# Performance work log

Measured on AMD Instinct MI355X. Metric: run time of the kernel, lower is better.

## Reference

```python
import jax, jax.numpy as jnp
import numpy as np

B, NG, H, G, T0, T1 = 4096, 3000, 6, 30, 500, 50  # batch, genes, hidden, genes/term, leaf terms, mid terms
EPS = 1e-5  # BatchNorm1d default eps


def _bn(x, gamma, beta):
    # training-mode BatchNorm1d: biased batch stats over the batch axis
    m = x.mean(axis=0)
    v = ((x - m) ** 2).mean(axis=0)
    return gamma * (x - m) / jnp.sqrt(v + EPS) + beta


def setup_inputs() -> dict:
    key = jax.random.key(0)
    ks = iter(jax.random.split(key, 32))
    rn = lambda shape, s=0.05: jax.random.normal(next(ks), shape, dtype=jnp.float32) * s
    return dict(
        cell_features=jax.random.normal(next(ks), (B, NG), dtype=jnp.float32),
        Wdg=rn((T0 + T1 + 1, G, NG)), bdg=rn((T0 + T1 + 1, G)),
        W0=rn((T0, H, G)), b0=rn((T0, H)), gam0=jnp.ones((T0, H), jnp.float32), bet0=jnp.zeros((T0, H), jnp.float32),
        aw0=rn((T0, H)), ab0=rn((T0,)), av0=rn((T0,)), ac0=rn((T0,)),
        W1=rn((T1, H, 10 * H + G)), b1=rn((T1, H)), gam1=jnp.ones((T1, H), jnp.float32), bet1=jnp.zeros((T1, H), jnp.float32),
        aw1=rn((T1, H)), ab1=rn((T1,)), av1=rn((T1,)), ac1=rn((T1,)),
        W2=rn((H, T1 * H + G)), b2=rn((H,)), gam2=jnp.ones((H,), jnp.float32), bet2=jnp.zeros((H,), jnp.float32),
        aw2=rn((H,)), ab2=rn(()), av2=rn(()), ac2=rn(()),
    )


def reference(cell_features, Wdg, bdg,
              W0, b0, gam0, bet0, aw0, ab0, av0, ac0,
              W1, b1, gam1, bet1, aw1, ab1, av1, ac1,
              W2, b2, gam2, bet2, aw2, ab2, av2, ac2):
    # direct_gene_layer for every term: Linear(ngene -> genes_per_term), no activation
    dg = jnp.einsum('bn,tgn->btg', cell_features, Wdg) + bdg  # [B, 551, G]
    # ---- layer 0 (leaves): input = direct gene output only ----
    z0 = jnp.tanh(jnp.einsum('btg,thg->bth', dg[:, :T0], W0) + b0)
    n0 = _bn(z0, gam0, bet0)                                   # [B, T0, H]
    aux0 = jnp.tanh(jnp.einsum('bth,th->bt', n0, aw0) + ab0) * av0 + ac0
    # ---- layer 1: term t's children are leaves [10t, 10t+10); concat children + direct genes ----
    in1 = jnp.concatenate([n0.reshape(B, T1, 10 * H), dg[:, T0:T0 + T1]], axis=-1)  # [B, T1, 90]
    z1 = jnp.tanh(jnp.einsum('bti,thi->bth', in1, W1) + b1)
    n1 = _bn(z1, gam1, bet1)                                   # [B, T1, H]
    aux1 = jnp.tanh(jnp.einsum('bth,th->bt', n1, aw1) + ab1) * av1 + ac1
    # ---- root: children = all mid terms + direct genes ----
    in2 = jnp.concatenate([n1.reshape(B, T1 * H), dg[:, -1]], axis=-1)  # [B, 330]
    z2 = jnp.tanh(in2 @ W2.T + b2)
    n2 = _bn(z2, gam2, bet2)                                   # [B, H]
    aux2 = jnp.tanh(n2 @ aw2 + ab2) * av2 + ac2                # [B]
    # flatten (aux_out_map, term_NN_out_map) into one array for a single comparable output
    aux_all = jnp.concatenate([aux0, aux1, aux2[:, None]], axis=1)              # [B, 551]
    nn_all = jnp.concatenate([n0.reshape(B, -1), n1.reshape(B, -1), n2], axis=1)  # [B, 551*H]
    return jnp.concatenate([aux_all, nn_all], axis=1)          # [B, 3857]
```

## Files before the change

kernel.cpp:

```cpp
#include <hip/hip_runtime.h>
#include <hip/hip_bf16.h>

#define BATCH 4096
#define NGENE 3000
#define HID   6
#define GPT   30
#define T0N   500
#define T1N   50
#define KP    3008
#define MROWS 4608
#define OUTW  3857
#define BNEPS 1e-5f

typedef __attribute__((ext_vector_type(8))) __bf16 bf16x8;
typedef __attribute__((ext_vector_type(4))) float f32x4;
typedef __attribute__((ext_vector_type(8))) unsigned short ushort8;

__device__ __forceinline__ unsigned short f2bf(float f) {
  unsigned int u = __builtin_bit_cast(unsigned int, f);
  u = (u + 0x7fffu + ((u >> 16) & 1u)) >> 16;
  return (unsigned short)u;
}

__device__ __forceinline__ void gload_lds16(const void* g, void* l) {
  __builtin_amdgcn_global_load_lds(
      (const __attribute__((address_space(1))) unsigned int*)g,
      (__attribute__((address_space(3))) unsigned int*)l, 16, 0, 0);
}

__device__ __forceinline__ void bn_ss(const float* __restrict__ st,
                                      const float* __restrict__ gam,
                                      const float* __restrict__ bet,
                                      int c, float& sc, float& sh) {
  float m = st[2 * c] * (1.f / BATCH);
  float v = st[2 * c + 1] * (1.f / BATCH) - m * m;
  sc = gam[c] * rsqrtf(v + BNEPS);
  sh = bet[c] - m * sc;
}

__global__ __launch_bounds__(256) void prep(
    const float* __restrict__ cell, const float* __restrict__ Wdg,
    const float* __restrict__ W0, const float* __restrict__ b0,
    const float* __restrict__ bdg,
    ushort8* __restrict__ cellb, unsigned short* __restrict__ abuf,
    float* __restrict__ bias, float* __restrict__ st) {
  int blk = blockIdx.x, tid = threadIdx.x;
  if (blk < 6016) {
    int idx = blk * 256 + tid;
    int r = idx / 376, c8 = idx - r * 376;
    int c = c8 * 8;
    ushort8 o = (ushort8)0;
    if (c < NGENE) {
      const float4* p = (const float4*)(cell + (size_t)r * NGENE + c);
      float4 a = p[0], b = p[1];
      o[0] = f2bf(a.x); o[1] = f2bf(a.y); o[2] = f2bf(a.z); o[3] = f2bf(a.w);
      o[4] = f2bf(b.x); o[5] = f2bf(b.y); o[6] = f2bf(b.z); o[7] = f2bf(b.w);
    }
    cellb[idx] = o;
  } else if (blk < 12016) {
    int bx = blk - 6016;
    int xb = bx % 12, t = bx / 12;
    int n = xb * 256 + tid;
    if (n >= KP) return;
    bool valid = n < NGENE;
    float x[GPT];
#pragma unroll
    for (int g = 0; g < GPT; ++g)
      x[g] = valid ? Wdg[((size_t)(t * GPT + g)) * NGENE + n] : 0.f;
#pragma unroll
    for (int h = 0; h < HID; ++h) {
      const float* w = W0 + (t * HID + h) * GPT;
      float s = 0.f;
#pragma unroll
      for (int g = 0; g < GPT; ++g) s += x[g] * w[g];
      abuf[((size_t)(t * HID + h)) * KP + n] = valid ? f2bf(s) : (unsigned short)0;
    }
  } else if (blk < 14264) {
    int idx = (blk - 12016) * 256 + tid;
    if (idx >= 1530 * 376) return;
    int r = idx / 376, c8 = idx - r * 376;
    int c = c8 * 8;
    ushort8 o = (ushort8)0;
    if (c < NGENE) {
      const float4* p = (const float4*)(Wdg + (size_t)(15000 + r) * NGENE + c);
      float4 a = p[0], b = p[1];
      o[0] = f2bf(a.x); o[1] = f2bf(a.y); o[2] = f2bf(a.z); o[3] = f2bf(a.w);
      o[4] = f2bf(b.x); o[5] = f2bf(b.y); o[6] = f2bf(b.z); o[7] = f2bf(b.w);
    }
    ((ushort8*)abuf)[(size_t)(3000 + r) * 376 + c8] = o;
  } else if (blk < 14379) {
    int idx = (blk - 14264) * 256 + tid;
    if (idx < 78 * 376) ((ushort8*)abuf)[(size_t)4530 * 376 + idx] = (ushort8)0;
  } else if (blk < 14397) {
    int idx = (blk - 14379) * 256 + tid;
    if (idx >= MROWS) return;
    float v = 0.f;
    if (idx < 3000) {
      int t = idx / HID;
      float s = b0[idx];
#pragma unroll
      for (int g = 0; g < GPT; ++g) s += W0[idx * GPT + g] * bdg[t * GPT + g];
      v = s;
    } else if (idx < 4530) {
      v = bdg[15000 + idx - 3000];
    }
    bias[idx] = v;
  } else {
    int idx = (blk - 14397) * 256 + tid;
    if (idx < 6612) st[idx] = 0.f;
  }
}

__global__ __launch_bounds__(256) void gemm_fused(
    const unsigned short* __restrict__ A,
    const unsigned short* __restrict__ Bt,
    const float* __restrict__ bias,
    float* __restrict__ C,
    float* __restrict__ st0) {
  __shared__ unsigned short smem[8192];
  const int tid  = threadIdx.x;
  const int wave = tid >> 6, lane = tid & 63;
  const int wm = wave >> 1, wn = wave & 1;
  const int quad = lane >> 4, fr = lane & 15;
  const int m0 = blockIdx.y * 128, n0 = blockIdx.x * 128;
  const int lrow = lane >> 2;
  const int lcol = (lane & 3) * 8;

  f32x4 acc[16] = {};

  for (int kt = 0; kt < KP / 32; ++kt) {
    const int k0 = kt * 32;
#pragma unroll
    for (int q = 0; q < 4; ++q) {
      int chunk = q * 4 + wave;
      const unsigned short* gsrc;
      if (chunk < 8) {
        int row = m0 + chunk * 16 + lrow;
        gsrc = A + (size_t)row * KP + k0 + lcol;
      } else {
        int row = n0 + (chunk - 8) * 16 + lrow;
        gsrc = Bt + (size_t)row * KP + k0 + lcol;
      }
      gload_lds16(gsrc, &smem[chunk * 512]);
    }
    asm volatile("s_waitcnt vmcnt(0)" ::: "memory");
    __syncthreads();

    bf16x8 af[4], bfr[4];
#pragma unroll
    for (int tm = 0; tm < 4; ++tm)
      af[tm] = ((const bf16x8*)smem)[((wm * 64 + tm * 16 + fr) * 32 + quad * 8) >> 3];
#pragma unroll
    for (int tn = 0; tn < 4; ++tn)
      bfr[tn] = ((const bf16x8*)smem)[(4096 + (wn * 64 + tn * 16 + fr) * 32 + quad * 8) >> 3];
#pragma unroll
    for (int tm = 0; tm < 4; ++tm)
#pragma unroll
      for (int tn = 0; tn < 4; ++tn)
        acc[tm * 4 + tn] = __builtin_amdgcn_mfma_f32_16x16x32_bf16(
            af[tm], bfr[tn], acc[tm * 4 + tn], 0, 0, 0);
    __syncthreads();
  }

#pragma unroll
  for (int tm = 0; tm < 4; ++tm) {
    const int mbase = m0 + wm * 64 + tm * 16 + quad * 4;
    float s1[4] = {0.f, 0.f, 0.f, 0.f}, s2[4] = {0.f, 0.f, 0.f, 0.f};
#pragma unroll
    for (int tn = 0; tn < 4; ++tn) {
      int n = n0 + wn * 64 + tn * 16 + fr;
#pragma unroll
      for (int r = 0; r < 4; ++r) {
        int m = mbase + r;
        float v = acc[tm * 4 + tn][r] + bias[m];
        if (m < 3000) {
          v = tanhf(v);
          s1[r] += v; s2[r] += v * v;
        }
        C[(size_t)m * BATCH + n] = v;
      }
    }
#pragma unroll
    for (int r = 0; r < 4; ++r) {
      int m = mbase + r;
      if (m < 3000) {
        float a = s1[r], q = s2[r];
        a += __shfl_xor(a, 1);  q += __shfl_xor(q, 1);
        a += __shfl_xor(a, 2);  q += __shfl_xor(q, 2);
        a += __shfl_xor(a, 4);  q += __shfl_xor(q, 4);
        a += __shfl_xor(a, 8);  q += __shfl_xor(q, 8);
        if (fr == 0) {
          atomicAdd(&st0[2 * m], a);
          atomicAdd(&st0[2 * m + 1], q);
        }
      }
    }
  }
}

__device__ void norm_emit_body(const float* __restrict__ zT, const float* __restrict__ st,
                               const float* __restrict__ gam, const float* __restrict__ bet,
                               float* __restrict__ out, int ncols, int outoff,
                               int xb, int yb) {
  __shared__ float tile[64][65];
  int lane = threadIdx.x & 63, w = threadIdx.x >> 6;
  int c0 = xb * 64, b0 = yb * 64;
#pragma unroll
  for (int i = 0; i < 16; ++i) {
    int cc = w * 16 + i, c = c0 + cc;
    float n = 0.f;
    if (c < ncols) {
      float sc, sh; bn_ss(st, gam, bet, c, sc, sh);
      n = zT[(size_t)c * BATCH + b0 + lane] * sc + sh;
    }
    tile[cc][lane] = n;
  }
  __syncthreads();
  int c = c0 + lane;
  if (c < ncols) {
#pragma unroll
    for (int i = 0; i < 16; ++i) {
      int rr = w * 16 + i;
      out[(size_t)(b0 + rr) * OUTW + outoff + c] = tile[lane][rr];
    }
  }
}

__global__ __launch_bounds__(256) void fused_l1(
    const float* __restrict__ C, const float* __restrict__ st0,
    const float* __restrict__ gam0, const float* __restrict__ bet0,
    const float* __restrict__ aw0, const float* __restrict__ ab0,
    const float* __restrict__ av0, const float* __restrict__ ac0,
    const float* __restrict__ W1, const float* __restrict__ b1,
    float* __restrict__ out, float* __restrict__ auxT,
    float* __restrict__ z1T, float* __restrict__ st1) {
  int blk = blockIdx.x;
  if (blk < 3008) {
    norm_emit_body(C, st0, gam0, bet0, out, 3000, 551, blk % 47, blk / 47);
  } else if (blk < 11008) {
    int b2 = blk - 3008;
    int lane = threadIdx.x & 63, tg = threadIdx.x >> 6;
    int t = (b2 % 125) * 4 + tg;
    int b = (b2 / 125) * 64 + lane;
    float s = ab0[t];
#pragma unroll
    for (int h = 0; h < HID; ++h) {
      int c = t * HID + h;
      float sc, sh; bn_ss(st0, gam0, bet0, c, sc, sh);
      s += (C[(size_t)c * BATCH + b] * sc + sh) * aw0[c];
    }
    auxT[(size_t)t * BATCH + b] = tanhf(s) * av0[t] + ac0[t];
  } else {
    int b3 = blk - 11008;
    int lane = threadIdx.x & 63, tg = threadIdx.x >> 6;
    int t = (b3 % 13) * 4 + tg;
    if (t >= T1N) return;
    int b = (b3 / 13) * 64 + lane;
    const float* dgm = C + (size_t)3000 * BATCH;
    float x[90];
#pragma unroll
    for (int j = 0; j < 60; ++j) {
      int c = t * 60 + j;
      float sc, sh; bn_ss(st0, gam0, bet0, c, sc, sh);
      x[j] = C[(size_t)c * BATCH + b] * sc + sh;
    }
#pragma unroll
    for (int g = 0; g < GPT; ++g)
      x[60 + g] = dgm[(size_t)(t * GPT + g) * BATCH + b];
#pragma unroll
    for (int h = 0; h < HID; ++h) {
      int c = t * HID + h;
      const float* w = W1 + c * 90;
      float s = b1[c];
#pragma unroll
      for (int i = 0; i < 90; ++i) s += x[i] * w[i];
      float z = tanhf(s);
      z1T[(size_t)c * BATCH + b] = z;
      float s1 = z, s2 = z * z;
#pragma unroll
      for (int off = 32; off > 0; off >>= 1) {
        s1 += __shfl_down(s1, off);
        s2 += __shfl_down(s2, off);
      }
      if (lane == 0) {
        atomicAdd(&st1[2 * c], s1);
        atomicAdd(&st1[2 * c + 1], s2);
      }
    }
  }
}

__global__ __launch_bounds__(256) void fused_l2(
    const float* __restrict__ C, const float* __restrict__ z1T,
    const float* __restrict__ st1,
    const float* __restrict__ gam1, const float* __restrict__ bet1,
    const float* __restrict__ aw1, const float* __restrict__ ab1,
    const float* __restrict__ av1, const float* __restrict__ ac1,
    const float* __restrict__ W2, const float* __restrict__ b2,
    float* __restrict__ out, float* __restrict__ auxT,
    float* __restrict__ z2T, float* __restrict__ st2) {
  int blk = blockIdx.x;
  if (blk < 320) {
    norm_emit_body(z1T, st1, gam1, bet1, out, 300, 3551, blk % 5, blk / 5);
  } else if (blk < 1152) {
    int b2 = blk - 320;
    int lane = threadIdx.x & 63, tg = threadIdx.x >> 6;
    int t = (b2 % 13) * 4 + tg;
    if (t >= T1N) return;
    int b = (b2 / 13) * 64 + lane;
    float s = ab1[t];
#pragma unroll
    for (int h = 0; h < HID; ++h) {
      int c = t * HID + h;
      float sc, sh; bn_ss(st1, gam1, bet1, c, sc, sh);
      s += (z1T[(size_t)c * BATCH + b] * sc + sh) * aw1[c];
    }
    auxT[(size_t)(T0N + t) * BATCH + b] = tanhf(s) * av1[t] + ac1[t];
  } else {
    int b = (blk - 1152) * 256 + threadIdx.x;
    int lane = threadIdx.x & 63;
    const float* dgr = C + (size_t)4500 * BATCH;
    float s[HID];
#pragma unroll
    for (int h = 0; h < HID; ++h) s[h] = b2[h];
    for (int c = 0; c < 300; ++c) {
      float sc, sh; bn_ss(st1, gam1, bet1, c, sc, sh);
      float n = z1T[(size_t)c * BATCH + b] * sc + sh;
#pragma unroll
      for (int h = 0; h < HID; ++h) s[h] += n * W2[h * 330 + c];
    }
#pragma unroll
    for (int g = 0; g < GPT; ++g) {
      float d = dgr[(size_t)g * BATCH + b];
#pragma unroll
      for (int h = 0; h < HID; ++h) s[h] += d * W2[h * 330 + 300 + g];
    }
#pragma unroll
    for (int h = 0; h < HID; ++h) {
      float z = tanhf(s[h]);
      z2T[(size_t)h * BATCH + b] = z;
      float s1 = z, s2 = z * z;
#pragma unroll
      for (int off = 32; off > 0; off >>= 1) {
        s1 += __shfl_down(s1, off);
        s2 += __shfl_down(s2, off);
      }
      if (lane == 0) {
        atomicAdd(&st2[2 * h], s1);
        atomicAdd(&st2[2 * h + 1], s2);
      }
    }
  }
}

__global__ __launch_bounds__(256) void fused_fin(
    const float* __restrict__ auxT, const float* __restrict__ z2T,
    const float* __restrict__ st2,
    const float* __restrict__ gam2, const float* __restrict__ bet2,
    const float* __restrict__ aw2, const float* __restrict__ ab2,
    const float* __restrict__ av2, const float* __restrict__ ac2,
    float* __restrict__ out) {
  int blk = blockIdx.x;
  if (blk < 576) {
    __shared__ float tile[64][65];
    int lane = threadIdx.x & 63, w = threadIdx.x >> 6;
    int c0 = (blk % 9) * 64, b0 = (blk / 9) * 64;
#pragma unroll
    for (int i = 0; i < 16; ++i) {
      int cc = w * 16 + i, c = c0 + cc;
      tile[cc][lane] = (c < 550) ? auxT[(size_t)c * BATCH + b0 + lane] : 0.f;
    }
    __syncthreads();
    int c = c0 + lane;
    if (c < 550) {
#pragma unroll
      for (int i = 0; i < 16; ++i) {
        int rr = w * 16 + i;
        out[(size_t)(b0 + rr) * OUTW + c] = tile[lane][rr];
      }
    }
  } else {
    int b = (blk - 576) * 256 + threadIdx.x;
    float s = ab2[0];
#pragma unroll
    for (int h = 0; h < HID; ++h) {
      float sc, sh; bn_ss(st2, gam2, bet2, h, sc, sh);
      float n = z2T[(size_t)h * BATCH + b] * sc + sh;
      out[(size_t)b * OUTW + 3851 + h] = n;
      s += n * aw2[h];
    }
    out[(size_t)b * OUTW + 550] = tanhf(s) * av2[0] + ac2[0];
  }
}

extern "C" void kernel_launch(void* const* d_in, const int* in_sizes, int n_in,
                              void* d_out, int out_size, void* d_ws, size_t ws_size,
                              hipStream_t stream) {
  (void)in_sizes; (void)n_in; (void)out_size; (void)ws_size;
  const float* cell = (const float*)d_in[0];
  const float* Wdg  = (const float*)d_in[1];
  const float* bdg  = (const float*)d_in[2];
  const float* W0   = (const float*)d_in[3];
  const float* b0   = (const float*)d_in[4];
  const float* gam0 = (const float*)d_in[5];
  const float* bet0 = (const float*)d_in[6];
  const float* aw0  = (const float*)d_in[7];
  const float* ab0  = (const float*)d_in[8];
  const float* av0  = (const float*)d_in[9];
  const float* ac0  = (const float*)d_in[10];
  const float* W1   = (const float*)d_in[11];
  const float* b1   = (const float*)d_in[12];
  const float* gam1 = (const float*)d_in[13];
  const float* bet1 = (const float*)d_in[14];
  const float* aw1  = (const float*)d_in[15];
  const float* ab1  = (const float*)d_in[16];
  const float* av1  = (const float*)d_in[17];
  const float* ac1  = (const float*)d_in[18];
  const float* W2   = (const float*)d_in[19];
  const float* b2   = (const float*)d_in[20];
  const float* gam2 = (const float*)d_in[21];
  const float* bet2 = (const float*)d_in[22];
  const float* aw2  = (const float*)d_in[23];
  const float* ab2  = (const float*)d_in[24];
  const float* av2  = (const float*)d_in[25];
  const float* ac2  = (const float*)d_in[26];
  float* out = (float*)d_out;

  char* ws = (char*)d_ws;
  unsigned short* cellb = (unsigned short*)(ws);
  unsigned short* abuf  = (unsigned short*)(ws + 24641536);
  float*          C     = (float*)(ws + 52363264);
  float*          z1T   = (float*)(ws + 127860736);
  float*          z2T   = (float*)(ws + 132775936);
  float*          st    = (float*)(ws + 132874240);
  float*          bias  = (float*)(ws + 132907008);
  float*          auxT  = (float*)(ws + 132925440);
  float* st0 = st, *st1 = st + 2 * 3000, *st2 = st + 2 * 3300;

  prep<<<14423, 256, 0, stream>>>(cell, Wdg, W0, b0, bdg,
                                  (ushort8*)cellb, abuf, bias, st);
  gemm_fused<<<dim3(32, 36), 256, 0, stream>>>(abuf, cellb, bias, C, st0);
  fused_l1<<<11840, 256, 0, stream>>>(C, st0, gam0, bet0, aw0, ab0, av0, ac0,
                                      W1, b1, out, auxT, z1T, st1);
  fused_l2<<<1168, 256, 0, stream>>>(C, z1T, st1, gam1, bet1, aw1, ab1, av1, ac1,
                                     W2, b2, out, auxT, z2T, st2);
  fused_fin<<<592, 256, 0, stream>>>(auxT, z2T, st2, gam2, bet2, aw2, ab2, av2, ac2,
                                     out);
}
```

Measured before the change: 699.4 us.

## Store layer-0 tanh activations as bf16 and compute BN stats in separate pass

The GEMM epilogue now writes the 3000 leaf-hidden tanh activations as bf16 into their own buffer and the direct-gene rows as fp32 into another, instead of one fp32 buffer. The in-epilogue shuffle reductions and atomics for BN statistics are removed, and a new colstats_b kernel computes per-column sums from the bf16 data. The layer-1 matvec is restructured to accumulate six outputs on the fly instead of holding a 90-element register array. This halves the traffic for the largest intermediate and trims register pressure, at the cost of an extra kernel launch and bf16 rounding of activations that feed BN and the output.

```diff
diff --git a/kernel.cpp b/kernel.cpp
--- a/kernel.cpp
+++ b/kernel.cpp
@@ -20,6 +20,11 @@
   unsigned int u = __builtin_bit_cast(unsigned int, f);
   u = (u + 0x7fffu + ((u >> 16) & 1u)) >> 16;
   return (unsigned short)u;
+}
+
+__device__ __forceinline__ float bf2f(unsigned short u) {
+  unsigned int x = ((unsigned int)u) << 16;
+  return __builtin_bit_cast(float, x);
 }
 
 __device__ __forceinline__ void gload_lds16(const void* g, void* l) {
@@ -115,8 +120,8 @@
     const unsigned short* __restrict__ A,
     const unsigned short* __restrict__ Bt,
     const float* __restrict__ bias,
-    float* __restrict__ C,
-    float* __restrict__ st0) {
+    unsigned short* __restrict__ z0b,
+    float* __restrict__ dgm) {
   __shared__ unsigned short smem[8192];
   const int tid  = threadIdx.x;
   const int wave = tid >> 6, lane = tid & 63;
@@ -164,70 +169,55 @@
 
 #pragma unroll
   for (int tm = 0; tm < 4; ++tm) {
-    const int mbase = m0 + wm * 64 + tm * 16 + quad * 4;
-    float s1[4] = {0.f, 0.f, 0.f, 0.f}, s2[4] = {0.f, 0.f, 0.f, 0.f};
 #pragma unroll
     for (int tn = 0; tn < 4; ++tn) {
       int n = n0 + wn * 64 + tn * 16 + fr;
 #pragma unroll
       for (int r = 0; r < 4; ++r) {
-        int m = mbase + r;
+        int m = m0 + wm * 64 + tm * 16 + quad * 4 + r;
         float v = acc[tm * 4 + tn][r] + bias[m];
         if (m < 3000) {
-          v = tanhf(v);
-          s1[r] += v; s2[r] += v * v;
+          z0b[(size_t)m * BATCH + n] = f2bf(tanhf(v));
+        } else {
+          dgm[(size_t)(m - 3000) * BATCH + n] = v;
         }
-        C[(size_t)m * BATCH + n] = v;
-      }
-    }
-#pragma unroll
-    for (int r = 0; r < 4; ++r) {
-      int m = mbase + r;
-      if (m < 3000) {
-        float a = s1[r], q = s2[r];
-        a += __shfl_xor(a, 1);  q += __shfl_xor(q, 1);
-        a += __shfl_xor(a, 2);  q += __shfl_xor(q, 2);
-        a += __shfl_xor(a, 4);  q += __shfl_xor(q, 4);
-        a += __shfl_xor(a, 8);  q += __shfl_xor(q, 8);
-        if (fr == 0) {
-          atomicAdd(&st0[2 * m], a);
-          atomicAdd(&st0[2 * m + 1], q);
-        }
-      }
-    }
-  }
-}
-
-__device__ void norm_emit_body(const float* __restrict__ zT, const float* __restrict__ st,
-                               const float* __restrict__ gam, const float* __restrict__ bet,
-                               float* __restrict__ out, int ncols, int outoff,
-                               int xb, int yb) {
-  __shared__ float tile[64][65];
+      }
+    }
+  }
+}
+
+__global__ __launch_bounds__(256) void colstats_b(const unsigned short* __restrict__ z0b,
+                                                  float* __restrict__ st0) {
+  int c = blockIdx.x;
+  const ushort8* p = (const ushort8*)(z0b + (size_t)c * BATCH);
+  float s = 0.f, q = 0.f;
+#pragma unroll
+  for (int it = 0; it < 2; ++it) {
+    ushort8 v8 = p[threadIdx.x + it * 256];
+#pragma unroll
+    for (int j = 0; j < 8; ++j) {
+      float f = bf2f(v8[j]);
+      s += f; q += f * f;
+    }
+  }
+#pragma unroll
+  for (int off = 32; off > 0; off >>= 1) {
+    s += __shfl_down(s, off);
+    q += __shfl_down(q, off);
+  }
+  __shared__ float ls[8];
   int lane = threadIdx.x & 63, w = threadIdx.x >> 6;
-  int c0 = xb * 64, b0 = yb * 64;
-#pragma unroll
-  for (int i = 0; i < 16; ++i) {
-    int cc = w * 16 + i, c = c0 + cc;
-    float n = 0.f;
-    if (c < ncols) {
-      float sc, sh; bn_ss(st, gam, bet, c, sc, sh);
-      n = zT[(size_t)c * BATCH + b0 + lane] * sc + sh;
-    }
-    tile[cc][lane] = n;
-  }
+  if (lane == 0) { ls[2 * w] = s; ls[2 * w + 1] = q; }
   __syncthreads();
-  int c = c0 + lane;
-  if (c < ncols) {
-#pragma unroll
-    for (int i = 0; i < 16; ++i) {
-      int rr = w * 16 + i;
-      out[(size_t)(b0 + rr) * OUTW + outoff + c] = tile[lane][rr];
-    }
+  if (threadIdx.x == 0) {
+    st0[2 * c]     = ls[0] + ls[2] + ls[4] + ls[6];
+    st0[2 * c + 1] = ls[1] + ls[3] + ls[5] + ls[7];
   }
 }
 
 __global__ __launch_bounds__(256) void fused_l1(
-    const float* __restrict__ C, const float* __restrict__ st0,
+    const unsigned short* __restrict__ z0b, const float* __restrict__ dgm,
+    const float* __restrict__ st0,
     const float* __restrict__ gam0, const float* __restrict__ bet0,
     const float* __restrict__ aw0, const float* __restrict__ ab0,
     const float* __restrict__ av0, const float* __restrict__ ac0,
@@ -236,7 +226,28 @@
     float* __restrict__ z1T, float* __restrict__ st1) {
   int blk = blockIdx.x;
   if (blk < 3008) {
-    norm_emit_body(C, st0, gam0, bet0, out, 3000, 551, blk % 47, blk / 47);
+    __shared__ float tile[64][65];
+    int lane = threadIdx.x & 63, w = threadIdx.x >> 6;
+    int c0 = (blk % 47) * 64, b0 = (blk / 47) * 64;
+#pragma unroll
+    for (int i = 0; i < 16; ++i) {
+      int cc = w * 16 + i, c = c0 + cc;
+      float n = 0.f;
+      if (c < 3000) {
+        float sc, sh; bn_ss(st0, gam0, bet0, c, sc, sh);
+        n = bf2f(z0b[(size_t)c * BATCH + b0 + lane]) * sc + sh;
+      }
+      tile[cc][lane] = n;
+    }
+    __syncthreads();
+    int c = c0 + lane;
+    if (c < 3000) {
+#pragma unroll
+      for (int i = 0; i < 16; ++i) {
+        int rr = w * 16 + i;
+        out[(size_t)(b0 + rr) * OUTW + 551 + c] = tile[lane][rr];
+      }
+    }
   } else if (blk < 11008) {
     int b2 = blk - 3008;
     int lane = threadIdx.x & 63, tg = threadIdx.x >> 6;
@@ -247,7 +258,7 @@
     for (int h = 0; h < HID; ++h) {
       int c = t * HID + h;
       float sc, sh; bn_ss(st0, gam0, bet0, c, sc, sh);
-      s += (C[(size_t)c * BATCH + b] * sc + sh) * aw0[c];
+      s += (bf2f(z0b[(size_t)c * BATCH + b]) * sc + sh) * aw0[c];
     }
     auxT[(size_t)t * BATCH + b] = tanhf(s) * av0[t] + ac0[t];
   } else {
@@ -256,25 +267,27 @@
     int t = (b3 % 13) * 4 + tg;
     if (t >= T1N) return;
     int b = (b3 / 13) * 64 + lane;
-    const float* dgm = C + (size_t)3000 * BATCH;
-    float x[90];
+    float s[HID];
+#pragma unroll
+    for (int h = 0; h < HID; ++h) s[h] = b1[t * HID + h];
 #pragma unroll
     for (int j = 0; j < 60; ++j) {
       int c = t * 60 + j;
       float sc, sh; bn_ss(st0, gam0, bet0, c, sc, sh);
-      x[j] = C[(size_t)c * BATCH + b] * sc + sh;
-    }
-#pragma unroll
-    for (int g = 0; g < GPT; ++g)
-      x[60 + g] = dgm[(size_t)(t * GPT + g) * BATCH + b];
+      float xv = bf2f(z0b[(size_t)c * BATCH + b]) * sc + sh;
+#pragma unroll
+      for (int h = 0; h < HID; ++h) s[h] += xv * W1[(t * HID + h) * 90 + j];
+    }
+#pragma unroll
+    for (int g = 0; g < GPT; ++g) {
+      float xv = dgm[(size_t)(t * GPT + g) * BATCH + b];
+#pragma unroll
+      for (int h = 0; h < HID; ++h) s[h] += xv * W1[(t * HID + h) * 90 + 60 + g];
+    }
 #pragma unroll
     for (int h = 0; h < HID; ++h) {
       int c = t * HID + h;
-      const float* w = W1 + c * 90;
-      float s = b1[c];
-#pragma unroll
-      for (int i = 0; i < 90; ++i) s += x[i] * w[i];
-      float z = tanhf(s);
+      float z = tanhf(s[h]);
       z1T[(size_t)c * BATCH + b] = z;
       float s1 = z, s2 = z * z;
 #pragma unroll
@@ -291,7 +304,7 @@
 }
 
 __global__ __launch_bounds__(256) void fused_l2(
-    const float* __restrict__ C, const float* __restrict__ z1T,
+    const float* __restrict__ dgm, const float* __restrict__ z1T,
     const float* __restrict__ st1,
     const float* __restrict__ gam1, const float* __restrict__ bet1,
     const float* __restrict__ aw1, const float* __restrict__ ab1,
@@ -301,13 +314,34 @@
     float* __restrict__ z2T, float* __restrict__ st2) {
   int blk = blockIdx.x;
   if (blk < 320) {
-    norm_emit_body(z1T, st1, gam1, bet1, out, 300, 3551, blk % 5, blk / 5);
+    __shared__ float tile[64][65];
+    int lane = threadIdx.x & 63, w = threadIdx.x >> 6;
+    int c0 = (blk % 5) * 64, b0 = (blk / 5) * 64;
+#pragma unroll
+    for (int i = 0; i < 16; ++i) {
+      int cc = w * 16 + i, c = c0 + cc;
+      float n = 0.f;
+      if (c < 300) {
+        float sc, sh; bn_ss(st1, gam1, bet1, c, sc, sh);
+        n = z1T[(size_t)c * BATCH + b0 + lane] * sc + sh;
+      }
+      tile[cc][lane] = n;
+    }
+    __syncthreads();
+    int c = c0 + lane;
+    if (c < 300) {
+#pragma unroll
+      for (int i = 0; i < 16; ++i) {
+        int rr = w * 16 + i;
+        out[(size_t)(b0 + rr) * OUTW + 3551 + c] = tile[lane][rr];
+      }
+    }
   } else if (blk < 1152) {
-    int b2 = blk - 320;
+    int b2_ = blk - 320;
     int lane = threadIdx.x & 63, tg = threadIdx.x >> 6;
-    int t = (b2 % 13) * 4 + tg;
+    int t = (b2_ % 13) * 4 + tg;
     if (t >= T1N) return;
-    int b = (b2 / 13) * 64 + lane;
+    int b = (b2_ / 13) * 64 + lane;
     float s = ab1[t];
 #pragma unroll
     for (int h = 0; h < HID; ++h) {
@@ -319,7 +353,7 @@
   } else {
     int b = (blk - 1152) * 256 + threadIdx.x;
     int lane = threadIdx.x & 63;
-    const float* dgr = C + (size_t)4500 * BATCH;
+    const float* dgr = dgm + (size_t)1500 * BATCH;
     float s[HID];
 #pragma unroll
     for (int h = 0; h < HID; ++h) s[h] = b2[h];
@@ -429,20 +463,22 @@
   char* ws = (char*)d_ws;
   unsigned short* cellb = (unsigned short*)(ws);
   unsigned short* abuf  = (unsigned short*)(ws + 24641536);
-  float*          C     = (float*)(ws + 52363264);
-  float*          z1T   = (float*)(ws + 127860736);
-  float*          z2T   = (float*)(ws + 132775936);
-  float*          st    = (float*)(ws + 132874240);
-  float*          bias  = (float*)(ws + 132907008);
-  float*          auxT  = (float*)(ws + 132925440);
+  unsigned short* z0b   = (unsigned short*)(ws + 52363264);
+  float*          dgm   = (float*)(ws + 76939264);
+  float*          z1T   = (float*)(ws + 103284736);
+  float*          z2T   = (float*)(ws + 108199936);
+  float*          st    = (float*)(ws + 108298240);
+  float*          bias  = (float*)(ws + 108331008);
+  float*          auxT  = (float*)(ws + 108349440);
   float* st0 = st, *st1 = st + 2 * 3000, *st2 = st + 2 * 3300;
 
   prep<<<14423, 256, 0, stream>>>(cell, Wdg, W0, b0, bdg,
                                   (ushort8*)cellb, abuf, bias, st);
-  gemm_fused<<<dim3(32, 36), 256, 0, stream>>>(abuf, cellb, bias, C, st0);
-  fused_l1<<<11840, 256, 0, stream>>>(C, st0, gam0, bet0, aw0, ab0, av0, ac0,
+  gemm_fused<<<dim3(32, 36), 256, 0, stream>>>(abuf, cellb, bias, z0b, dgm);
+  colstats_b<<<3000, 256, 0, stream>>>(z0b, st0);
+  fused_l1<<<11840, 256, 0, stream>>>(z0b, dgm, st0, gam0, bet0, aw0, ab0, av0, ac0,
                                       W1, b1, out, auxT, z1T, st1);
-  fused_l2<<<1168, 256, 0, stream>>>(C, z1T, st1, gam1, bet1, aw1, ab1, av1, ac1,
+  fused_l2<<<1168, 256, 0, stream>>>(dgm, z1T, st1, gam1, bet1, aw1, ab1, av1, ac1,
                                      W2, b2, out, auxT, z2T, st2);
   fused_fin<<<592, 256, 0, stream>>>(auxT, z2T, st2, gam2, bet2, aw2, ab2, av2, ac2,
                                      out);
```

Measured after the change: 758.5 us. 8.4% more time.
